# Kernel optimization log

Measured on AMD Instinct MI355X. Metric: run time of the kernel, lower is better.

## Reference

```python
import jax, jax.numpy as jnp
import numpy as np

HID = 128; H = 8; D = HID // H; L = 2; IN = 128; OUT = 32
ND = 20000; NF = 50000; E = 400000
SQRT_D = float(np.sqrt(D))
LN_EPS = 1e-5


def setup_inputs() -> dict:
    key = jax.random.key(0)
    ks = jax.random.split(key, 16)
    s = 1.0 / np.sqrt(HID)
    n = lambda k, sh, sc=1.0: jax.random.normal(k, sh, jnp.float32) * sc
    return dict(
        x_device=n(ks[0], (ND, IN)),
        x_feature=n(ks[1], (NF, IN)),
        e_df_src=jax.random.randint(ks[2], (E,), 0, ND),
        e_df_dst=jax.random.randint(ks[3], (E,), 0, NF),
        e_fd_src=jax.random.randint(ks[4], (E,), 0, NF),
        e_fd_dst=jax.random.randint(ks[5], (E,), 0, ND),
        W_dev_in=n(ks[6], (IN, HID), s), b_dev_in=jnp.zeros((HID,), jnp.float32),
        W_feat_in=n(ks[7], (IN, HID), s), b_feat_in=jnp.zeros((HID,), jnp.float32),
        Wk=n(ks[8], (L, 2, HID, HID), s), bk=jnp.zeros((L, 2, HID), jnp.float32),
        Wq=n(ks[9], (L, 2, HID, HID), s), bq=jnp.zeros((L, 2, HID), jnp.float32),
        Wv=n(ks[10], (L, 2, HID, HID), s), bv=jnp.zeros((L, 2, HID), jnp.float32),
        a_rel=n(ks[11], (L, 2, H, D, D), 1.0 / np.sqrt(D)),
        m_rel=n(ks[12], (L, 2, H, D, D), 1.0 / np.sqrt(D)),
        p_rel=jnp.ones((L, 2, H), jnp.float32),
        Wa=n(ks[13], (L, 2, HID, HID), s), ba=jnp.zeros((L, 2, HID), jnp.float32),
        skip=jnp.ones((L, 2), jnp.float32),
        ln_g=jnp.ones((L, 2, HID), jnp.float32), ln_b=jnp.zeros((L, 2, HID), jnp.float32),
        W_out=n(ks[14], (HID, OUT), s), b_out=jnp.zeros((OUT,), jnp.float32),
    )


def _layer_norm(x, g, b):
    m = x.mean(-1, keepdims=True)
    v = ((x - m) ** 2).mean(-1, keepdims=True)
    return (x - m) * jax.lax.rsqrt(v + LN_EPS) * g + b


def _edge_agg(q_dst, k_src, v_src, a_r, m_r, p_r, src, dst, n_dst):
    # per-edge-type relation transforms of source k/v: [N_src,H,D]
    kt = jnp.einsum('nhd,hde->nhe', k_src, a_r)
    vt = jnp.einsum('nhd,hde->nhe', v_src, m_r)
    # per-edge attention logits [E,H], scaled by relation prior
    logit = (q_dst[dst] * kt[src]).sum(-1) * p_r / SQRT_D
    # segment softmax over incoming edges of each dst node (per edge type)
    mx = jax.ops.segment_max(logit, dst, num_segments=n_dst)
    ex = jnp.exp(logit - mx[dst])
    sm = jax.ops.segment_sum(ex, dst, num_segments=n_dst)
    alpha = ex / (sm[dst] + 1e-16)
    # attention-weighted message scatter-sum -> [n_dst,H,D]
    return jax.ops.segment_sum(vt[src] * alpha[..., None], dst, num_segments=n_dst)


def _forward(x_device, x_feature, W_dev_in, b_dev_in, W_feat_in, b_feat_in,
             Wk, bk, Wq, bq, Wv, bv, a_rel, m_rel, p_rel, Wa, ba, skip,
             ln_g, ln_b, W_out, b_out, e_df_src, e_df_dst, e_fd_src, e_fd_dst):
    x_d = jax.nn.relu(x_device @ W_dev_in + b_dev_in)
    x_f = jax.nn.relu(x_feature @ W_feat_in + b_feat_in)
    for l in range(L):
        xs = (x_d, x_f)  # node-type 0 = device, 1 = feature
        k = [(xs[t] @ Wk[l, t] + bk[l, t]).reshape(-1, H, D) for t in range(2)]
        q = [(xs[t] @ Wq[l, t] + bq[l, t]).reshape(-1, H, D) for t in range(2)]
        v = [(xs[t] @ Wv[l, t] + bv[l, t]).reshape(-1, H, D) for t in range(2)]
        # edge type 0: device -> feature ; edge type 1: feature -> device
        agg_f = _edge_agg(q[1], k[0], v[0], a_rel[l, 0], m_rel[l, 0], p_rel[l, 0],
                          e_df_src, e_df_dst, NF)
        agg_d = _edge_agg(q[0], k[1], v[1], a_rel[l, 1], m_rel[l, 1], p_rel[l, 1],
                          e_fd_src, e_fd_dst, ND)
        new = []
        for t, agg in ((0, agg_d), (1, agg_f)):
            o = jax.nn.gelu(agg.reshape(-1, HID), approximate=False) @ Wa[l, t] + ba[l, t]
            sk = jax.nn.sigmoid(skip[l, t])
            o = sk * o + (1.0 - sk) * xs[t]              # HGTConv skip
            new.append(_layer_norm(xs[t] + o, ln_g[l, t], ln_b[l, t]))  # wrapper residual+LN (dropout=identity in eval)
        x_d, x_f = new
    return x_d @ W_out + b_out


def reference(x_device, x_feature, e_df_src, e_df_dst, e_fd_src, e_fd_dst,
              W_dev_in, b_dev_in, W_feat_in, b_feat_in, Wk, bk, Wq, bq, Wv, bv,
              a_rel, m_rel, p_rel, Wa, ba, skip, ln_g, ln_b, W_out, b_out):
    return _forward(x_device, x_feature, W_dev_in, b_dev_in, W_feat_in, b_feat_in,
                    Wk, bk, Wq, bq, Wv, bv, a_rel, m_rel, p_rel, Wa, ba, skip,
                    ln_g, ln_b, W_out, b_out, e_df_src, e_df_dst, e_fd_src, e_fd_dst)
```

## Files before the change

### kernel.cpp

```cpp
#include <hip/hip_runtime.h>
#include <math.h>

#define ND 20000
#define NF 50000
#define NE 400000
#define NT (NF + ND)

typedef __attribute__((ext_vector_type(8))) short short8;
typedef __attribute__((ext_vector_type(4))) float f32x4;
typedef unsigned short us;

static __device__ __forceinline__ us f2bf(float f) {
    unsigned u = __builtin_bit_cast(unsigned, f);
    u += 0x7FFF + ((u >> 16) & 1);
    return (us)(u >> 16);
}
static __device__ __forceinline__ float bf2f(us h) {
    return __builtin_bit_cast(float, (unsigned)h << 16);
}
static __device__ __forceinline__ float bflo(unsigned u) {
    return __builtin_bit_cast(float, u << 16);
}
static __device__ __forceinline__ float bfhi(unsigned u) {
    return __builtin_bit_cast(float, u & 0xFFFF0000u);
}
static __device__ __forceinline__ float gelu_f(float x) {
    return 0.5f * x * (1.0f + erff(x * 0.70710678118654752f));
}

__global__ void prep_all(const float* __restrict__ W_dev_in, const float* __restrict__ W_feat_in,
                         const float* __restrict__ Wq, const float* __restrict__ Wk,
                         const float* __restrict__ Wv, const float* __restrict__ Wa,
                         const float* __restrict__ b_dev_in, const float* __restrict__ b_feat_in,
                         const float* __restrict__ bq, const float* __restrict__ bk,
                         const float* __restrict__ bv, const float* __restrict__ ba,
                         const float* __restrict__ a_rel, const float* __restrict__ m_rel,
                         const float* __restrict__ p_rel,
                         us* __restrict__ WT, float* __restrict__ B_all) {
    int idx = blockIdx.x * 256 + threadIdx.x;
    if (idx < 18 * 16384) {
        int k = idx & 127, c = (idx >> 7) & 127, id = idx >> 14;
        float val;
        if (id == 0) val = W_dev_in[k * 128 + c];
        else if (id == 1) val = W_feat_in[k * 128 + c];
        else if (id < 6) val = Wq[(id - 2) * 16384 + k * 128 + c];
        else if (id < 10) {
            int lt = id - 6, h = c >> 4, e = c & 15;
            const float* A = a_rel + (lt * 8 + h) * 256;
            const float* Ws = Wk + lt * 16384 + k * 128 + h * 16;
            float sm = 0.f;
            #pragma unroll
            for (int d = 0; d < 16; ++d) sm += Ws[d] * A[d * 16 + e];
            val = sm * p_rel[lt * 8 + h] * 0.25f;
        } else if (id < 14) {
            int lt = id - 10, h = c >> 4, e = c & 15;
            const float* A = m_rel + (lt * 8 + h) * 256;
            const float* Ws = Wv + lt * 16384 + k * 128 + h * 16;
            float sm = 0.f;
            #pragma unroll
            for (int d = 0; d < 16; ++d) sm += Ws[d] * A[d * 16 + e];
            val = sm;
        } else val = Wa[(id - 14) * 16384 + k * 128 + c];
        WT[(size_t)id * 16384 + (((c * 128 + k)) ^ ((c & 7) << 3))] = f2bf(val);
    } else {
        int j = idx - 18 * 16384;
        if (j >= 18 * 128) return;
        int c = j & 127, id = j >> 7;
        float v;
        if (id == 0) v = b_dev_in[c];
        else if (id == 1) v = b_feat_in[c];
        else if (id < 6) v = bq[(id - 2) * 128 + c];
        else if (id < 10) {
            int lt = id - 6, h = c >> 4, e = c & 15;
            const float* A = a_rel + (lt * 8 + h) * 256;
            const float* bs = bk + lt * 128 + h * 16;
            float sm = 0.f;
            #pragma unroll
            for (int d = 0; d < 16; ++d) sm += bs[d] * A[d * 16 + e];
            v = sm * p_rel[lt * 8 + h] * 0.25f;
        } else if (id < 14) {
            int lt = id - 10, h = c >> 4, e = c & 15;
            const float* A = m_rel + (lt * 8 + h) * 256;
            const float* bs = bv + lt * 128 + h * 16;
            float sm = 0.f;
            #pragma unroll
            for (int d = 0; d < 16; ++d) sm += bs[d] * A[d * 16 + e];
            v = sm;
        } else v = ba[(id - 14) * 128 + c];
        B_all[j] = v;
    }
}

template<int AF32, int RELU, int LNF>
__global__ __launch_bounds__(256) void mfma_gemm2(
    const void* __restrict__ X0, const void* __restrict__ X1,
    const us* __restrict__ WT0, const float* __restrict__ Ball,
    us* __restrict__ Y0, us* __restrict__ Y1,
    int N0, int N1, int GB0, int widbase,
    us* __restrict__ X0w, us* __restrict__ X1w,
    const float* __restrict__ skipv, const float* __restrict__ lng,
    const float* __restrict__ lnb) {
    __shared__ us Wlds[16384];
    const int type = (blockIdx.x >= (unsigned)GB0) ? 1 : 0;
    const int bx = blockIdx.x - (type ? GB0 : 0);
    const int N = type ? N1 : N0;
    const void* Xv = type ? X1 : X0;
    const int wid = widbase + type + 4 * blockIdx.y;
    const us* WT = WT0 + (size_t)wid * 16384;
    const float* bias = Ball + wid * 128;

    const int lane = threadIdx.x & 63;
    const int wave = threadIdx.x >> 6;
    const int row_base = bx * 128 + wave * 32;
    const int l15 = lane & 15, lg = lane >> 4;
    const int kbase = lg * 8;

    {
        const char* gsrc = (const char*)WT + wave * 8192 + lane * 16;
        char* ldst = (char*)Wlds + wave * 8192;
        #pragma unroll
        for (int i = 0; i < 8; ++i) {
            __builtin_amdgcn_global_load_lds(
                (const __attribute__((address_space(1))) void*)(gsrc + i * 1024),
                (__attribute__((address_space(3))) void*)(ldst + i * 1024),
                16, 0, 0);
        }
    }

    short8 a[2][4];
    #pragma unroll
    for (int mf = 0; mf < 2; ++mf) {
        int r = row_base + mf * 16 + l15;
        r = r < N ? r : N - 1;
        if (AF32) {
            const float* Xf = (const float*)Xv + (size_t)r * 128;
            #pragma unroll
            for (int kf = 0; kf < 4; ++kf) {
                float4 lo = *(const float4*)(Xf + kf * 32 + kbase);
                float4 hi = *(const float4*)(Xf + kf * 32 + kbase + 4);
                short8 t;
                t[0] = (short)f2bf(lo.x); t[1] = (short)f2bf(lo.y);
                t[2] = (short)f2bf(lo.z); t[3] = (short)f2bf(lo.w);
                t[4] = (short)f2bf(hi.x); t[5] = (short)f2bf(hi.y);
                t[6] = (short)f2bf(hi.z); t[7] = (short)f2bf(hi.w);
                a[mf][kf] = t;
            }
        } else {
            const us* Xb = (const us*)Xv + (size_t)r * 128;
            #pragma unroll
            for (int kf = 0; kf < 4; ++kf)
                a[mf][kf] = *(const short8*)(Xb + kf * 32 + kbase);
        }
    }

    __syncthreads();

    f32x4 acc[2][8];
    #pragma unroll
    for (int mf = 0; mf < 2; ++mf)
        #pragma unroll
        for (int cf = 0; cf < 8; ++cf) acc[mf][cf] = (f32x4){0.f, 0.f, 0.f, 0.f};

    const unsigned swz = (unsigned)((l15 & 7) << 4);
    #pragma unroll
    for (int cf = 0; cf < 8; ++cf) {
        const unsigned rowbyte = (unsigned)((cf * 16 + l15) * 256 + kbase * 2);
        #pragma unroll
        for (int kf = 0; kf < 4; ++kf) {
            short8 b = *(const short8*)((const char*)Wlds + ((rowbyte + kf * 64) ^ swz));
            acc[0][cf] = __builtin_amdgcn_mfma_f32_16x16x32_bf16(a[0][kf], b, acc[0][cf], 0, 0, 0);
            acc[1][cf] = __builtin_amdgcn_mfma_f32_16x16x32_bf16(a[1][kf], b, acc[1][cf], 0, 0, 0);
        }
    }

    float bval[8];
    #pragma unroll
    for (int cf = 0; cf < 8; ++cf) bval[cf] = bias[cf * 16 + l15];

    if (LNF) {
        const int lt = widbase - 14 + type;
        float sk = 1.f / (1.f + __expf(-skipv[lt]));
        float gv[8], bv2[8];
        #pragma unroll
        for (int cf = 0; cf < 8; ++cf) {
            gv[cf]  = lng[(size_t)lt * 128 + cf * 16 + l15];
            bv2[cf] = lnb[(size_t)lt * 128 + cf * 16 + l15];
        }
        us* xw = type ? X1w : X0w;
        #pragma unroll
        for (int mf = 0; mf < 2; ++mf)
            #pragma unroll
            for (int r = 0; r < 4; ++r) {
                int grow = row_base + mf * 16 + lg * 4 + r;
                if (grow >= N) continue;
                float t[8];
                float sum = 0.f;
                #pragma unroll
                for (int cf = 0; cf < 8; ++cf) {
                    float o = acc[mf][cf][r] + bval[cf];
                    float x = bf2f(xw[(size_t)grow * 128 + cf * 16 + l15]);
                    t[cf] = (2.f - sk) * x + sk * o;
                    sum += t[cf];
                }
                sum += __shfl_xor(sum, 1); sum += __shfl_xor(sum, 2);
                sum += __shfl_xor(sum, 4); sum += __shfl_xor(sum, 8);
                float mean = sum * (1.0f / 128.0f);
                float vs = 0.f;
                #pragma unroll
                for (int cf = 0; cf < 8; ++cf) { t[cf] -= mean; vs += t[cf] * t[cf]; }
                vs += __shfl_xor(vs, 1); vs += __shfl_xor(vs, 2);
                vs += __shfl_xor(vs, 4); vs += __shfl_xor(vs, 8);
                float inv = rsqrtf(vs * (1.0f / 128.0f) + 1e-5f);
                #pragma unroll
                for (int cf = 0; cf < 8; ++cf)
                    xw[(size_t)grow * 128 + cf * 16 + l15] = f2bf(t[cf] * inv * gv[cf] + bv2[cf]);
            }
        return;
    }

    us* Yp = (type ? Y1 : Y0) + (size_t)blockIdx.y * N * 128;
    #pragma unroll
    for (int mf = 0; mf < 2; ++mf)
        #pragma unroll
        for (int r = 0; r < 4; ++r) {
            int grow = row_base + mf * 16 + lg * 4 + r;
            if (grow >= N) continue;
            #pragma unroll
            for (int cf = 0; cf < 8; ++cf) {
                float v = acc[mf][cf][r] + bval[cf];
                if (RELU) v = fmaxf(v, 0.f);
                Yp[(size_t)grow * 128 + cf * 16 + l15] = f2bf(v);
            }
        }
}

__global__ __launch_bounds__(256) void gemm_out_k(
    const us* __restrict__ X, const float* __restrict__ W,
    const float* __restrict__ bias, float* __restrict__ Y, int N) {
    __shared__ float Ws[128 * 32];
    __shared__ float Xs[8][128];
    const int tid = threadIdx.x;
    const int row0 = blockIdx.x * 8;
    #pragma unroll
    for (int it = 0; it < 16; ++it) Ws[it * 256 + tid] = W[it * 256 + tid];
    #pragma unroll
    for (int it = 0; it < 2; ++it) {
        int idx = it * 256 + tid;
        int rr = idx >> 6, kp = idx & 63;
        int gr = row0 + rr;
        unsigned u = (gr < N) ? *(const unsigned*)(X + (size_t)gr * 128 + kp * 2) : 0u;
        Xs[rr][kp * 2]     = bflo(u);
        Xs[rr][kp * 2 + 1] = bfhi(u);
    }
    __syncthreads();
    const int rr = tid >> 5, c = tid & 31;
    float acc = bias[c];
    #pragma unroll 8
    for (int k = 0; k < 128; ++k)
        acc = fmaf(Xs[rr][k], Ws[k * 32 + c], acc);
    int gr = row0 + rr;
    if (gr < N) Y[(size_t)gr * 32 + c] = acc;
}

#define EDGE_STEP(kc, vc, pidx)                                        \
    {                                                                  \
        float part = qv[0] * bflo(kc.x);                               \
        part = fmaf(qv[1], bfhi(kc.x), part);                          \
        part = fmaf(qv[2], bflo(kc.y), part);                          \
        part = fmaf(qv[3], bfhi(kc.y), part);                          \
        part = fmaf(qv[4], bflo(kc.z), part);                          \
        part = fmaf(qv[5], bfhi(kc.z), part);                          \
        part = fmaf(qv[6], bflo(kc.w), part);                          \
        part = fmaf(qv[7], bfhi(kc.w), part);                          \
        part += __shfl_xor(part, 1);                                   \
        float w = ((pidx) < p1) ? __expf(part) : 0.f;                  \
        s += w;                                                        \
        a[0] = fmaf(w, bflo(vc.x), a[0]);                              \
        a[1] = fmaf(w, bfhi(vc.x), a[1]);                              \
        a[2] = fmaf(w, bflo(vc.y), a[2]);                              \
        a[3] = fmaf(w, bfhi(vc.y), a[3]);                              \
        a[4] = fmaf(w, bflo(vc.z), a[4]);                              \
        a[5] = fmaf(w, bfhi(vc.z), a[5]);                              \
        a[6] = fmaf(w, bflo(vc.w), a[6]);                              \
        a[7] = fmaf(w, bfhi(vc.w), a[7]);                              \
    }

__global__ __launch_bounds__(256) void edge_agg2(
    const us* __restrict__ qf, const us* __restrict__ qd,
    const us* __restrict__ ktf, const us* __restrict__ ktd,
    const us* __restrict__ vtf, const us* __restrict__ vtd,
    const int* __restrict__ rs, const int* __restrict__ esrc,
    us* __restrict__ aggf, us* __restrict__ aggd) {
    int g = (blockIdx.x * 256 + threadIdx.x) >> 4;
    int li = threadIdx.x & 15;
    if (g >= NT) return;
    const us *q, *kt, *vt; us* agg; int dst;
    if (g < NF) { dst = g;      q = qf; kt = ktd; vt = vtd; agg = aggf; }
    else        { dst = g - NF; q = qd; kt = ktf; vt = vtf; agg = aggd; }

    uint4 qb = *(const uint4*)(q + (size_t)dst * 128 + li * 8);
    float qv[8];
    qv[0] = bflo(qb.x); qv[1] = bfhi(qb.x);
    qv[2] = bflo(qb.y); qv[3] = bfhi(qb.y);
    qv[4] = bflo(qb.z); qv[5] = bfhi(qb.z);
    qv[6] = bflo(qb.w); qv[7] = bfhi(qb.w);

    const int p0 = rs[g], p1 = rs[g + 1];
    float s = 0.f;
    float a[8];
    #pragma unroll
    for (int j = 0; j < 8; ++j) a[j] = 0.f;

    const size_t loff = (size_t)li * 8;
    uint4 kA0, vA0, kA1, vA1, kB0, vB0, kB1, vB1;
    int sN0, sN1, sN2, sN3;

    if (p0 < p1) {
        const int last = p1 - 1;
        int i0 = p0, i1 = min(p0 + 1, last), i2 = min(p0 + 2, last), i3 = min(p0 + 3, last);
        int s0 = esrc[i0], s1 = esrc[i1], s2 = esrc[i2], s3 = esrc[i3];
        kA0 = *(const uint4*)(kt + (size_t)s0 * 128 + loff);
        vA0 = *(const uint4*)(vt + (size_t)s0 * 128 + loff);
        kA1 = *(const uint4*)(kt + (size_t)s1 * 128 + loff);
        vA1 = *(const uint4*)(vt + (size_t)s1 * 128 + loff);
        kB0 = *(const uint4*)(kt + (size_t)s2 * 128 + loff);
        vB0 = *(const uint4*)(vt + (size_t)s2 * 128 + loff);
        kB1 = *(const uint4*)(kt + (size_t)s3 * 128 + loff);
        vB1 = *(const uint4*)(vt + (size_t)s3 * 128 + loff);
        sN0 = esrc[min(p0 + 4, last)];
        sN1 = esrc[min(p0 + 5, last)];
        sN2 = esrc[min(p0 + 6, last)];
        sN3 = esrc[min(p0 + 7, last)];

        for (int p = p0; p < p1; p += 4) {
            const int lastc = last;
            EDGE_STEP(kA0, vA0, p);
            EDGE_STEP(kA1, vA1, p + 1);
            kA0 = *(const uint4*)(kt + (size_t)sN0 * 128 + loff);
            vA0 = *(const uint4*)(vt + (size_t)sN0 * 128 + loff);
            kA1 = *(const uint4*)(kt + (size_t)sN1 * 128 + loff);
            vA1 = *(const uint4*)(vt + (size_t)sN1 * 128 + loff);
            sN0 = esrc[min(p + 8, lastc)];
            sN1 = esrc[min(p + 9, lastc)];
            EDGE_STEP(kB0, vB0, p + 2);
            EDGE_STEP(kB1, vB1, p + 3);
            kB0 = *(const uint4*)(kt + (size_t)sN2 * 128 + loff);
            vB0 = *(const uint4*)(vt + (size_t)sN2 * 128 + loff);
            kB1 = *(const uint4*)(kt + (size_t)sN3 * 128 + loff);
            vB1 = *(const uint4*)(vt + (size_t)sN3 * 128 + loff);
            sN2 = esrc[min(p + 10, lastc)];
            sN3 = esrc[min(p + 11, lastc)];
        }
    }

    float r = 1.0f / (s + 1e-16f);
    unsigned o[4];
    #pragma unroll
    for (int j = 0; j < 4; ++j) {
        us lo = f2bf(gelu_f(a[2 * j] * r));
        us hi = f2bf(gelu_f(a[2 * j + 1] * r));
        o[j] = (unsigned)lo | ((unsigned)hi << 16);
    }
    *(uint4*)(agg + (size_t)dst * 128 + li * 8) = make_uint4(o[0], o[1], o[2], o[3]);
}

__global__ void k_count2(const int* __restrict__ dA, const int* __restrict__ dB,
                         int* __restrict__ cnt) {
    int i = blockIdx.x * 256 + threadIdx.x;
    if (i < NE) atomicAdd(&cnt[dA[i]], 1);
    else if (i < 2 * NE) atomicAdd(&cnt[NF + dB[i - NE]], 1);
}

__global__ void k_scan_partial(const int* __restrict__ cnt, int* __restrict__ part, int n) {
    __shared__ int sd[256];
    int t = threadIdx.x;
    int base = blockIdx.x * 1024 + t * 4;
    int s = 0;
    #pragma unroll
    for (int j = 0; j < 4; ++j) { int i = base + j; if (i < n) s += cnt[i]; }
    sd[t] = s; __syncthreads();
    for (int off = 128; off > 0; off >>= 1) {
        if (t < off) sd[t] += sd[t + off];
        __syncthreads();
    }
    if (t == 0) part[blockIdx.x] = sd[0];
}

__global__ void k_scan_small(int* part, int nb, int* row_start, int n) {
    if (threadIdx.x == 0 && blockIdx.x == 0) {
        int run = 0;
        for (int i = 0; i < nb; ++i) { int v = part[i]; part[i] = run; run += v; }
        row_start[n] = run;
    }
}

__global__ void k_scan_final(int* __restrict__ cnt, const int* __restrict__ part,
                             int* __restrict__ row_start, int n) {
    __shared__ int sd[256];
    int t = threadIdx.x;
    int base = blockIdx.x * 1024 + t * 4;
    int v[4]; int s = 0;
    #pragma unroll
    for (int j = 0; j < 4; ++j) { int i = base + j; v[j] = (i < n) ? cnt[i] : 0; s += v[j]; }
    sd[t] = s; __syncthreads();
    for (int off = 1; off < 256; off <<= 1) {
        int add = (t >= off) ? sd[t - off] : 0;
        __syncthreads();
        sd[t] += add;
        __syncthreads();
    }
    int excl = part[blockIdx.x] + sd[t] - s;
    #pragma unroll
    for (int j = 0; j < 4; ++j) {
        int i = base + j;
        if (i < n) { row_start[i] = excl; cnt[i] = excl; }
        excl += v[j];
    }
}

__global__ void k_fill2(const int* __restrict__ sA, const int* __restrict__ dA,
                        const int* __restrict__ sB, const int* __restrict__ dB,
                        int* __restrict__ cursor, int* __restrict__ esrc) {
    int i = blockIdx.x * 256 + threadIdx.x;
    if (i < NE) {
        int p = atomicAdd(&cursor[dA[i]], 1);
        esrc[p] = sA[i];
    } else if (i < 2 * NE) {
        int j = i - NE;
        int p = atomicAdd(&cursor[NF + dB[j]], 1);
        esrc[p] = sB[j];
    }
}

extern "C" void kernel_launch(void* const* d_in, const int* in_sizes, int n_in,
                              void* d_out, int out_size, void* d_ws, size_t ws_size,
                              hipStream_t stream) {
    const float* x_device = (const float*)d_in[0];
    const float* x_feature = (const float*)d_in[1];
    const int* e_df_src = (const int*)d_in[2];
    const int* e_df_dst = (const int*)d_in[3];
    const int* e_fd_src = (const int*)d_in[4];
    const int* e_fd_dst = (const int*)d_in[5];
    const float* W_dev_in = (const float*)d_in[6];
    const float* b_dev_in = (const float*)d_in[7];
    const float* W_feat_in = (const float*)d_in[8];
    const float* b_feat_in = (const float*)d_in[9];
    const float* Wk = (const float*)d_in[10];
    const float* bk = (const float*)d_in[11];
    const float* Wq = (const float*)d_in[12];
    const float* bq = (const float*)d_in[13];
    const float* Wv = (const float*)d_in[14];
    const float* bv = (const float*)d_in[15];
    const float* a_rel = (const float*)d_in[16];
    const float* m_rel = (const float*)d_in[17];
    const float* p_rel = (const float*)d_in[18];
    const float* Wa = (const float*)d_in[19];
    const float* ba = (const float*)d_in[20];
    const float* skip = (const float*)d_in[21];
    const float* ln_g = (const float*)d_in[22];
    const float* ln_b = (const float*)d_in[23];
    const float* W_out = (const float*)d_in[24];
    const float* b_out = (const float*)d_in[25];

    char* ws = (char*)d_ws;
    size_t off = 0;
    auto alloc = [&](size_t bytes) -> void* {
        void* p = ws + off;
        off = (off + bytes + 255) & ~(size_t)255;
        return p;
    };
    us* xd     = (us*)alloc((size_t)ND * 128 * 2);
    us* xf     = (us*)alloc((size_t)NF * 128 * 2);
    us* qkv_d  = (us*)alloc((size_t)3 * ND * 128 * 2);
    us* qkv_f  = (us*)alloc((size_t)3 * NF * 128 * 2);
    us* agg_d  = (us*)alloc((size_t)ND * 128 * 2);
    us* agg_f  = (us*)alloc((size_t)NF * 128 * 2);
    us* WT     = (us*)alloc((size_t)18 * 16384 * 2);
    float* B_all = (float*)alloc(18 * 128 * 4);
    int* cnt    = (int*)alloc((size_t)NT * 4);
    int* rs     = (int*)alloc((size_t)(NT + 1) * 4);
    int* esrc   = (int*)alloc((size_t)(2 * NE + 8) * 4);
    int* part   = (int*)alloc(128 * 4);

    hipMemsetAsync(cnt, 0, (size_t)NT * 4, stream);
    k_count2<<<(2 * NE + 255) / 256, 256, 0, stream>>>(e_df_dst, e_fd_dst, cnt);
    int nb = (NT + 1023) / 1024;
    k_scan_partial<<<nb, 256, 0, stream>>>(cnt, part, NT);
    k_scan_small<<<1, 64, 0, stream>>>(part, nb, rs, NT);
    k_scan_final<<<nb, 256, 0, stream>>>(cnt, part, rs, NT);
    k_fill2<<<(2 * NE + 255) / 256, 256, 0, stream>>>(e_df_src, e_df_dst,
                                                      e_fd_src, e_fd_dst, cnt, esrc);

    prep_all<<<(18 * 16384 + 18 * 128 + 255) / 256, 256, 0, stream>>>(
        W_dev_in, W_feat_in, Wq, Wk, Wv, Wa,
        b_dev_in, b_feat_in, bq, bk, bv, ba,
        a_rel, m_rel, p_rel, WT, B_all);

    const int GBD = (ND + 127) / 128, GBF = (NF + 127) / 128;

    mfma_gemm2<1, 1, 0><<<dim3(GBD + GBF, 1), 256, 0, stream>>>(
        x_device, x_feature, WT, B_all, xd, xf, ND, NF, GBD, 0,
        nullptr, nullptr, nullptr, nullptr, nullptr);

    for (int l = 0; l < 2; ++l) {
        mfma_gemm2<0, 0, 0><<<dim3(GBD + GBF, 3), 256, 0, stream>>>(
            xd, xf, WT, B_all, qkv_d, qkv_f, ND, NF, GBD, 2 + l * 2,
            nullptr, nullptr, nullptr, nullptr, nullptr);

        edge_agg2<<<((NT * 16) + 255) / 256, 256, 0, stream>>>(
            qkv_f, qkv_d,
            qkv_f + (size_t)NF * 128, qkv_d + (size_t)ND * 128,
            qkv_f + (size_t)2 * NF * 128, qkv_d + (size_t)2 * ND * 128,
            rs, esrc, agg_f, agg_d);

        mfma_gemm2<0, 0, 1><<<dim3(GBD + GBF, 1), 256, 0, stream>>>(
            agg_d, agg_f, WT, B_all, nullptr, nullptr, ND, NF, GBD, 14 + l * 2,
            xd, xf, skip, ln_g, ln_b);
    }

    gemm_out_k<<<(ND + 7) / 8, 256, 0, stream>>>(xd, W_out, b_out, (float*)d_out, ND);
}
```

Measured before the change: 315.1 us.

## Interleave K/V per source node, split edge aggregation, fuse count with weight prep

The QKV projection now writes K and V side by side in one 256-wide row per node, so each gathered source in edge aggregation reads K and V from adjacent memory instead of two separate arrays. Edge aggregation is split into two launches, one per destination type, which removes the per-thread branch on node type. The edge-count kernel and the weight-prep kernel are merged into one launch, and the serial single-thread partial scan is replaced by a parallel shared-memory scan. Together these aim to improve gather locality and cut launch overhead, at the cost of an extra edge-aggregation launch and a more branchy GEMM epilogue.

```diff
diff --git a/kernel.cpp b/kernel.cpp
--- a/kernel.cpp
+++ b/kernel.cpp
@@ -28,16 +28,24 @@
     return 0.5f * x * (1.0f + erff(x * 0.70710678118654752f));
 }
 
-__global__ void prep_all(const float* __restrict__ W_dev_in, const float* __restrict__ W_feat_in,
-                         const float* __restrict__ Wq, const float* __restrict__ Wk,
-                         const float* __restrict__ Wv, const float* __restrict__ Wa,
-                         const float* __restrict__ b_dev_in, const float* __restrict__ b_feat_in,
-                         const float* __restrict__ bq, const float* __restrict__ bk,
-                         const float* __restrict__ bv, const float* __restrict__ ba,
-                         const float* __restrict__ a_rel, const float* __restrict__ m_rel,
-                         const float* __restrict__ p_rel,
-                         us* __restrict__ WT, float* __restrict__ B_all) {
-    int idx = blockIdx.x * 256 + threadIdx.x;
+__global__ void k_count_prep(const int* __restrict__ dA, const int* __restrict__ dB,
+                             int* __restrict__ cnt, int EB,
+                             const float* __restrict__ W_dev_in, const float* __restrict__ W_feat_in,
+                             const float* __restrict__ Wq, const float* __restrict__ Wk,
+                             const float* __restrict__ Wv, const float* __restrict__ Wa,
+                             const float* __restrict__ b_dev_in, const float* __restrict__ b_feat_in,
+                             const float* __restrict__ bq, const float* __restrict__ bk,
+                             const float* __restrict__ bv, const float* __restrict__ ba,
+                             const float* __restrict__ a_rel, const float* __restrict__ m_rel,
+                             const float* __restrict__ p_rel,
+                             us* __restrict__ WT, float* __restrict__ B_all) {
+    if ((int)blockIdx.x < EB) {
+        int i = blockIdx.x * 256 + threadIdx.x;
+        if (i < NE) atomicAdd(&cnt[dA[i]], 1);
+        else if (i < 2 * NE) atomicAdd(&cnt[NF + dB[i - NE]], 1);
+        return;
+    }
+    int idx = (blockIdx.x - EB) * 256 + threadIdx.x;
     if (idx < 18 * 16384) {
         int k = idx & 127, c = (idx >> 7) & 127, id = idx >> 14;
         float val;
@@ -91,13 +99,13 @@
     }
 }
 
-template<int AF32, int RELU, int LNF>
+template<int MODE, int AF32, int RELU>
 __global__ __launch_bounds__(256) void mfma_gemm2(
     const void* __restrict__ X0, const void* __restrict__ X1,
     const us* __restrict__ WT0, const float* __restrict__ Ball,
     us* __restrict__ Y0, us* __restrict__ Y1,
     int N0, int N1, int GB0, int widbase,
-    us* __restrict__ X0w, us* __restrict__ X1w,
+    us* __restrict__ K0, us* __restrict__ K1,
     const float* __restrict__ skipv, const float* __restrict__ lng,
     const float* __restrict__ lnb) {
     __shared__ us Wlds[16384];
@@ -177,7 +185,7 @@
     #pragma unroll
     for (int cf = 0; cf < 8; ++cf) bval[cf] = bias[cf * 16 + l15];
 
-    if (LNF) {
+    if (MODE == 2) {
         const int lt = widbase - 14 + type;
         float sk = 1.f / (1.f + __expf(-skipv[lt]));
         float gv[8], bv2[8];
@@ -186,7 +194,7 @@
             gv[cf]  = lng[(size_t)lt * 128 + cf * 16 + l15];
             bv2[cf] = lnb[(size_t)lt * 128 + cf * 16 + l15];
         }
-        us* xw = type ? X1w : X0w;
+        us* xw = type ? K1 : K0;
         #pragma unroll
         for (int mf = 0; mf < 2; ++mf)
             #pragma unroll
@@ -218,7 +226,6 @@
         return;
     }
 
-    us* Yp = (type ? Y1 : Y0) + (size_t)blockIdx.y * N * 128;
     #pragma unroll
     for (int mf = 0; mf < 2; ++mf)
         #pragma unroll
@@ -229,7 +236,13 @@
             for (int cf = 0; cf < 8; ++cf) {
                 float v = acc[mf][cf][r] + bval[cf];
                 if (RELU) v = fmaxf(v, 0.f);
-                Yp[(size_t)grow * 128 + cf * 16 + l15] = f2bf(v);
+                us val = f2bf(v);
+                int col = cf * 16 + l15;
+                if (MODE == 0 || blockIdx.y == 0) {
+                    (type ? Y1 : Y0)[(size_t)grow * 128 + col] = val;
+                } else {
+                    (type ? K1 : K0)[(size_t)grow * 256 + (blockIdx.y - 1) * 128 + col] = val;
+                }
             }
         }
 }
@@ -285,18 +298,14 @@
         a[7] = fmaf(w, bfhi(vc.w), a[7]);                              \
     }
 
-__global__ __launch_bounds__(256) void edge_agg2(
-    const us* __restrict__ qf, const us* __restrict__ qd,
-    const us* __restrict__ ktf, const us* __restrict__ ktd,
-    const us* __restrict__ vtf, const us* __restrict__ vtd,
+__global__ __launch_bounds__(256) void edge_agg3(
+    const us* __restrict__ q, const us* __restrict__ kv,
     const int* __restrict__ rs, const int* __restrict__ esrc,
-    us* __restrict__ aggf, us* __restrict__ aggd) {
-    int g = (blockIdx.x * 256 + threadIdx.x) >> 4;
+    us* __restrict__ agg, int n_dst, int goff) {
+    int dst = (blockIdx.x * 256 + threadIdx.x) >> 4;
     int li = threadIdx.x & 15;
-    if (g >= NT) return;
-    const us *q, *kt, *vt; us* agg; int dst;
-    if (g < NF) { dst = g;      q = qf; kt = ktd; vt = vtd; agg = aggf; }
-    else        { dst = g - NF; q = qd; kt = ktf; vt = vtf; agg = aggd; }
+    if (dst >= n_dst) return;
+    int g = dst + goff;
 
     uint4 qb = *(const uint4*)(q + (size_t)dst * 128 + li * 8);
     float qv[8];
@@ -319,14 +328,14 @@
         const int last = p1 - 1;
         int i0 = p0, i1 = min(p0 + 1, last), i2 = min(p0 + 2, last), i3 = min(p0 + 3, last);
         int s0 = esrc[i0], s1 = esrc[i1], s2 = esrc[i2], s3 = esrc[i3];
-        kA0 = *(const uint4*)(kt + (size_t)s0 * 128 + loff);
-        vA0 = *(const uint4*)(vt + (size_t)s0 * 128 + loff);
-        kA1 = *(const uint4*)(kt + (size_t)s1 * 128 + loff);
-        vA1 = *(const uint4*)(vt + (size_t)s1 * 128 + loff);
-        kB0 = *(const uint4*)(kt + (size_t)s2 * 128 + loff);
-        vB0 = *(const uint4*)(vt + (size_t)s2 * 128 + loff);
-        kB1 = *(const uint4*)(kt + (size_t)s3 * 128 + loff);
-        vB1 = *(const uint4*)(vt + (size_t)s3 * 128 + loff);
+        kA0 = *(const uint4*)(kv + (size_t)s0 * 256 + loff);
+        vA0 = *(const uint4*)(kv + (size_t)s0 * 256 + 128 + loff);
+        kA1 = *(const uint4*)(kv + (size_t)s1 * 256 + loff);
+        vA1 = *(const uint4*)(kv + (size_t)s1 * 256 + 128 + loff);
+        kB0 = *(const uint4*)(kv + (size_t)s2 * 256 + loff);
+        vB0 = *(const uint4*)(kv + (size_t)s2 * 256 + 128 + loff);
+        kB1 = *(const uint4*)(kv + (size_t)s3 * 256 + loff);
+        vB1 = *(const uint4*)(kv + (size_t)s3 * 256 + 128 + loff);
         sN0 = esrc[min(p0 + 4, last)];
         sN1 = esrc[min(p0 + 5, last)];
         sN2 = esrc[min(p0 + 6, last)];
@@ -336,18 +345,18 @@
             const int lastc = last;
             EDGE_STEP(kA0, vA0, p);
             EDGE_STEP(kA1, vA1, p + 1);
-            kA0 = *(const uint4*)(kt + (size_t)sN0 * 128 + loff);
-            vA0 = *(const uint4*)(vt + (size_t)sN0 * 128 + loff);
-            kA1 = *(const uint4*)(kt + (size_t)sN1 * 128 + loff);
-            vA1 = *(const uint4*)(vt + (size_t)sN1 * 128 + loff);
+            kA0 = *(const uint4*)(kv + (size_t)sN0 * 256 + loff);
+            vA0 = *(const uint4*)(kv + (size_t)sN0 * 256 + 128 + loff);
+            kA1 = *(const uint4*)(kv + (size_t)sN1 * 256 + loff);
+            vA1 = *(const uint4*)(kv + (size_t)sN1 * 256 + 128 + loff);
             sN0 = esrc[min(p + 8, lastc)];
             sN1 = esrc[min(p + 9, lastc)];
             EDGE_STEP(kB0, vB0, p + 2);
             EDGE_STEP(kB1, vB1, p + 3);
-            kB0 = *(const uint4*)(kt + (size_t)sN2 * 128 + loff);
-            vB0 = *(const uint4*)(vt + (size_t)sN2 * 128 + loff);
-            kB1 = *(const uint4*)(kt + (size_t)sN3 * 128 + loff);
-            vB1 = *(const uint4*)(vt + (size_t)sN3 * 128 + loff);
+            kB0 = *(const uint4*)(kv + (size_t)sN2 * 256 + loff);
+            vB0 = *(const uint4*)(kv + (size_t)sN2 * 256 + 128 + loff);
+            kB1 = *(const uint4*)(kv + (size_t)sN3 * 256 + loff);
+            vB1 = *(const uint4*)(kv + (size_t)sN3 * 256 + 128 + loff);
             sN2 = esrc[min(p + 10, lastc)];
             sN3 = esrc[min(p + 11, lastc)];
         }
@@ -362,13 +371,6 @@
         o[j] = (unsigned)lo | ((unsigned)hi << 16);
     }
     *(uint4*)(agg + (size_t)dst * 128 + li * 8) = make_uint4(o[0], o[1], o[2], o[3]);
-}
-
-__global__ void k_count2(const int* __restrict__ dA, const int* __restrict__ dB,
-                         int* __restrict__ cnt) {
-    int i = blockIdx.x * 256 + threadIdx.x;
-    if (i < NE) atomicAdd(&cnt[dA[i]], 1);
-    else if (i < 2 * NE) atomicAdd(&cnt[NF + dB[i - NE]], 1);
 }
 
 __global__ void k_scan_partial(const int* __restrict__ cnt, int* __restrict__ part, int n) {
@@ -386,12 +388,20 @@
     if (t == 0) part[blockIdx.x] = sd[0];
 }
 
-__global__ void k_scan_small(int* part, int nb, int* row_start, int n) {
-    if (threadIdx.x == 0 && blockIdx.x == 0) {
-        int run = 0;
-        for (int i = 0; i < nb; ++i) { int v = part[i]; part[i] = run; run += v; }
-        row_start[n] = run;
-    }
+__global__ void k_scan_small(int* __restrict__ part, int nb,
+                             int* __restrict__ row_start, int n) {
+    __shared__ int sd[128];
+    int t = threadIdx.x;
+    int v = (t < nb) ? part[t] : 0;
+    sd[t] = v; __syncthreads();
+    for (int off = 1; off < 128; off <<= 1) {
+        int add = (t >= off) ? sd[t - off] : 0;
+        __syncthreads();
+        sd[t] += add;
+        __syncthreads();
+    }
+    if (t < nb) part[t] = sd[t] - v;
+    if (t == 127) row_start[n] = sd[127];
 }
 
 __global__ void k_scan_final(int* __restrict__ cnt, const int* __restrict__ part,
@@ -471,8 +481,10 @@
     };
     us* xd     = (us*)alloc((size_t)ND * 128 * 2);
     us* xf     = (us*)alloc((size_t)NF * 128 * 2);
-    us* qkv_d  = (us*)alloc((size_t)3 * ND * 128 * 2);
-    us* qkv_f  = (us*)alloc((size_t)3 * NF * 128 * 2);
+    us* q_d    = (us*)alloc((size_t)ND * 128 * 2);
+    us* q_f    = (us*)alloc((size_t)NF * 128 * 2);
+    us* kv_d   = (us*)alloc((size_t)ND * 256 * 2);
+    us* kv_f   = (us*)alloc((size_t)NF * 256 * 2);
     us* agg_d  = (us*)alloc((size_t)ND * 128 * 2);
     us* agg_f  = (us*)alloc((size_t)NF * 128 * 2);
     us* WT     = (us*)alloc((size_t)18 * 16384 * 2);
@@ -482,38 +494,40 @@
     int* esrc   = (int*)alloc((size_t)(2 * NE + 8) * 4);
     int* part   = (int*)alloc(128 * 4);
 
+    const int EB = (2 * NE + 255) / 256;
+    const int PB = (18 * 16384 + 18 * 128 + 255) / 256;
+
     hipMemsetAsync(cnt, 0, (size_t)NT * 4, stream);
-    k_count2<<<(2 * NE + 255) / 256, 256, 0, stream>>>(e_df_dst, e_fd_dst, cnt);
+    k_count_prep<<<EB + PB, 256, 0, stream>>>(
+        e_df_dst, e_fd_dst, cnt, EB,
+        W_dev_in, W_feat_in, Wq, Wk, Wv, Wa,
+        b_dev_in, b_feat_in, bq, bk, bv, ba,
+        a_rel, m_rel, p_rel, WT, B_all);
+
     int nb = (NT + 1023) / 1024;
     k_scan_partial<<<nb, 256, 0, stream>>>(cnt, part, NT);
-    k_scan_small<<<1, 64, 0, stream>>>(part, nb, rs, NT);
+    k_scan_small<<<1, 128, 0, stream>>>(part, nb, rs, NT);
     k_scan_final<<<nb, 256, 0, stream>>>(cnt, part, rs, NT);
     k_fill2<<<(2 * NE + 255) / 256, 256, 0, stream>>>(e_df_src, e_df_dst,
                                                       e_fd_src, e_fd_dst, cnt, esrc);
 
-    prep_all<<<(18 * 16384 + 18 * 128 + 255) / 256, 256, 0, stream>>>(
-        W_dev_in, W_feat_in, Wq, Wk, Wv, Wa,
-        b_dev_in, b_feat_in, bq, bk, bv, ba,
-        a_rel, m_rel, p_rel, WT, B_all);
-
     const int GBD = (ND + 127) / 128, GBF = (NF + 127) / 128;
 
-    mfma_gemm2<1, 1, 0><<<dim3(GBD + GBF, 1), 256, 0, stream>>>(
+    mfma_gemm2<0, 1, 1><<<dim3(GBD + GBF, 1), 256, 0, stream>>>(
         x_device, x_feature, WT, B_all, xd, xf, ND, NF, GBD, 0,
         nullptr, nullptr, nullptr, nullptr, nullptr);
 
     for (int l = 0; l < 2; ++l) {
-        mfma_gemm2<0, 0, 0><<<dim3(GBD + GBF, 3), 256, 0, stream>>>(
-            xd, xf, WT, B_all, qkv_d, qkv_f, ND, NF, GBD, 2 + l * 2,
-            nullptr, nullptr, nullptr, nullptr, nullptr);
-
-        edge_agg2<<<((NT * 16) + 255) / 256, 256, 0, stream>>>(
-            qkv_f, qkv_d,
-            qkv_f + (size_t)NF * 128, qkv_d + (size_t)ND * 128,
-            qkv_f + (size_t)2 * NF * 128, qkv_d + (size_t)2 * ND * 128,
-            rs, esrc, agg_f, agg_d);
-
-        mfma_gemm2<0, 0, 1><<<dim3(GBD + GBF, 1), 256, 0, stream>>>(
+        mfma_gemm2<1, 0, 0><<<dim3(GBD + GBF, 3), 256, 0, stream>>>(
+            xd, xf, WT, B_all, q_d, q_f, ND, NF, GBD, 2 + l * 2,
+            kv_d, kv_f, nullptr, nullptr, nullptr);
+
+        edge_agg3<<<((NF * 16) + 255) / 256, 256, 0, stream>>>(
+            q_f, kv_d, rs, esrc, agg_f, NF, 0);
+        edge_agg3<<<((ND * 16) + 255) / 256, 256, 0, stream>>>(
+            q_d, kv_f, rs, esrc, agg_d, ND, NF);
+
+        mfma_gemm2<2, 0, 0><<<dim3(GBD + GBF, 1), 256, 0, stream>>>(
             agg_d, agg_f, WT, B_all, nullptr, nullptr, ND, NF, GBD, 14 + l * 2,
             xd, xf, skip, ln_g, ln_b);
     }
```

After: 320.4 us. Within noise of the previous version (+1.7%).
